# Performance work log

Measured on AMD Instinct MI355X. Metric: run time of the kernel, lower is better.

## Reference

```python
import jax, jax.numpy as jnp
import numpy as np

B, L, C = 256, 196, 768      # batch, tokens (14x14 grid), token_dim
K = 2048                      # codebook size (num_tokens)
H = W = 14                    # h = int(sqrt(L)), w = L // h


def setup_inputs() -> dict:
    key = jax.random.key(0)
    k1, k2, k3 = jax.random.split(key, 3)
    in_feas = jax.random.normal(k1, (B, L, C), dtype=jnp.float32)
    codebook = jax.random.normal(k2, (K, C), dtype=jnp.float32)
    # Conv1d(in=C, out=1, kernel=3, padding=1, bias=False) weight: [1, C, 3]
    att_w = jax.random.normal(k3, (1, C, 3), dtype=jnp.float32) * 0.02
    return {"in_feas": in_feas, "codebook": codebook, "att_w": att_w}


def reference(in_feas, codebook, att_w):
    b, l, c = in_feas.shape
    flat = in_feas.reshape(-1, c)  # [B*L, C]

    # --- SOHO visual-dictionary (VQ) nearest-neighbour lookup ---
    d = (jnp.sum(flat * flat, axis=1, keepdims=True)
         - 2.0 * flat @ codebook.T
         + jnp.sum(codebook * codebook, axis=1)[None, :])  # [B*L, K]
    encoding_indices = jnp.argmin(d, axis=1)               # [B*L] int
    quantized = codebook[encoding_indices]                 # [B*L, C]
    # straight-through estimator: output = x + sg(q - x)
    vd_outputs = flat + jax.lax.stop_gradient(quantized - flat)

    idx_out = encoding_indices.reshape(-1, H, W)

    # --- attention branch (att=True, not_plus=False) ---
    # Conv1d(C->1, k=3, pad=1) applied to each token as a length-1 sequence:
    # only the center tap att_w[0, :, 1] multiplies real data (neighbors are
    # zero padding), so the conv reduces to a dot with the center weights.
    att = jax.nn.relu(vd_outputs @ att_w[0, :, 1])         # [B*L]
    att_mask = jax.nn.softmax(att.reshape(b, l, 1), axis=1)  # softmax over L

    vd_outputs = vd_outputs.reshape(b, l, c)
    out_feas = vd_outputs + in_feas * att_mask
    return out_feas, idx_out
```

## Files before the change

kernel.cpp:

```cpp
#include <hip/hip_runtime.h>

#define B_ 256
#define L_ 196
#define C_ 768
#define K_ 2048
#define BL_ 50176

typedef __attribute__((ext_vector_type(8))) short bf16x8;
typedef __attribute__((ext_vector_type(4))) float f32x4;

typedef const __attribute__((address_space(1))) void gas_void;
typedef __attribute__((address_space(3))) void las_void;

__device__ __forceinline__ unsigned short f2bf(float f) {
  unsigned u = __builtin_bit_cast(unsigned, f);
  u = u + 0x7FFFu + ((u >> 16) & 1u);
  return (unsigned short)(u >> 16);
}

__device__ __forceinline__ unsigned fmono(float f) {
  unsigned u = __builtin_bit_cast(unsigned, f);
  return u ^ ((unsigned)((int)u >> 31) | 0x80000000u);
}

__global__ __launch_bounds__(256) void precompute_kernel(
    const float* __restrict__ cb, const float* __restrict__ attw,
    unsigned short* __restrict__ cbb, double* __restrict__ norms64,
    float* __restrict__ norms32, float* __restrict__ ac) {
  int wave = threadIdx.x >> 6;
  int lane = threadIdx.x & 63;
  int k = blockIdx.x * 4 + wave;
  const float* row = cb + (size_t)k * C_;
  double n = 0.0, a = 0.0;
  for (int c = lane; c < C_; c += 64) {
    float v = row[c];
    cbb[(size_t)k * C_ + c] = f2bf(v);
    n = fma((double)v, (double)v, n);
    a = fma((double)v, (double)attw[c * 3 + 1], a);
  }
  for (int off = 32; off > 0; off >>= 1) {
    n += __shfl_down(n, off);
    a += __shfl_down(a, off);
  }
  if (lane == 0) {
    norms64[k] = n;
    norms32[k] = (float)n;
    ac[k] = (a > 0.0) ? (float)a : 0.0f;
  }
}

__global__ __launch_bounds__(256) void convert_kernel(
    const float* __restrict__ x, unsigned short* __restrict__ xb) {
  int i = blockIdx.x * 256 + threadIdx.x;
  float4 v = ((const float4*)x)[i];
  uint2 w;
  w.x = (unsigned)f2bf(v.x) | ((unsigned)f2bf(v.y) << 16);
  w.y = (unsigned)f2bf(v.z) | ((unsigned)f2bf(v.w) << 16);
  ((uint2*)xb)[i] = w;
}

__global__ __launch_bounds__(256) void phase1_kernel(
    const unsigned short* __restrict__ xb,
    const unsigned short* __restrict__ cbb,
    const float* __restrict__ norms32, unsigned* __restrict__ ws_cand) {
  __shared__ unsigned short As[128 * 64];
  __shared__ unsigned short Bs[128 * 64];
  __shared__ float norms_s[128];
  __shared__ unsigned cands_s[128][8];

  int tid = threadIdx.x;
  int mblk = blockIdx.x, nblk = blockIdx.y;
  size_t row0 = (size_t)mblk * 128;
  int code0 = nblk * 128;

  if (tid < 128) norms_s[tid] = norms32[code0 + tid];

  int w = tid >> 6, l = tid & 63;
  int wm = w >> 1, wn = w & 1;
  int col16 = l & 15, quad = l >> 4;

  f32x4 acc[4][4];
#pragma unroll
  for (int mt = 0; mt < 4; ++mt)
#pragma unroll
    for (int nt = 0; nt < 4; ++nt) acc[mt][nt] = (f32x4){0.f, 0.f, 0.f, 0.f};

  int srow = 32 * w + (l >> 3);
  int sslot = (l & 7) ^ (l >> 3);
  const unsigned short* asrc = xb + (row0 + srow) * (size_t)C_ + sslot * 8;
  const unsigned short* bsrc =
      cbb + (size_t)(code0 + srow) * C_ + sslot * 8;
  char* alds = (char*)As + w * 4096;
  char* blds = (char*)Bs + w * 4096;

  for (int kt = 0; kt < 12; ++kt) {
    __syncthreads();
    int koff = kt * 64;
#pragma unroll
    for (int i = 0; i < 4; ++i) {
      __builtin_amdgcn_global_load_lds((gas_void*)(asrc + koff + i * 8 * C_),
                                       (las_void*)(alds + i * 1024), 16, 0, 0);
      __builtin_amdgcn_global_load_lds((gas_void*)(bsrc + koff + i * 8 * C_),
                                       (las_void*)(blds + i * 1024), 16, 0, 0);
    }
    __syncthreads();
#pragma unroll
    for (int ks = 0; ks < 2; ++ks) {
      int slot = (ks * 4 + quad) ^ (col16 & 7);
      bf16x8 af[4], bf[4];
#pragma unroll
      for (int mt = 0; mt < 4; ++mt) {
        int row = wm * 64 + mt * 16 + col16;
        af[mt] = *(const bf16x8*)((const char*)As + row * 128 + slot * 16);
      }
#pragma unroll
      for (int nt = 0; nt < 4; ++nt) {
        int row = wn * 64 + nt * 16 + col16;
        bf[nt] = *(const bf16x8*)((const char*)Bs + row * 128 + slot * 16);
      }
#pragma unroll
      for (int mt = 0; mt < 4; ++mt)
#pragma unroll
        for (int nt = 0; nt < 4; ++nt)
          acc[mt][nt] = __builtin_amdgcn_mfma_f32_16x16x32_bf16(
              af[mt], bf[nt], acc[mt][nt], 0, 0, 0);
    }
  }

#pragma unroll
  for (int mt = 0; mt < 4; ++mt) {
#pragma unroll
    for (int r = 0; r < 4; ++r) {
      unsigned keys[4];
#pragma unroll
      for (int nt = 0; nt < 4; ++nt) {
        int codel = wn * 64 + nt * 16 + col16;
        float d = fmaf(-2.0f, acc[mt][nt][r], norms_s[codel]);
        keys[nt] = (fmono(d) & 0xFFFFF800u) | (unsigned)(code0 + codel);
      }
      unsigned win[3];
#pragma unroll
      for (int rnd = 0; rnd < 3; ++rnd) {
        unsigned mn = min(min(keys[0], keys[1]), min(keys[2], keys[3]));
        mn = min(mn, (unsigned)__shfl_xor((int)mn, 1));
        mn = min(mn, (unsigned)__shfl_xor((int)mn, 2));
        mn = min(mn, (unsigned)__shfl_xor((int)mn, 4));
        mn = min(mn, (unsigned)__shfl_xor((int)mn, 8));
        win[rnd] = mn;
#pragma unroll
        for (int nt = 0; nt < 4; ++nt)
          if (keys[nt] == mn) keys[nt] = 0xFFFFFFFFu;
      }
      if (col16 == 0) {
        int t = wm * 64 + mt * 16 + quad * 4 + r;
        cands_s[t][wn * 3 + 0] = win[0];
        cands_s[t][wn * 3 + 1] = win[1];
        cands_s[t][wn * 3 + 2] = win[2];
      }
    }
  }
  __syncthreads();
  for (int i = tid; i < 128 * 6; i += 256) {
    int t = i / 6;
    int j = i - t * 6;
    ws_cand[(row0 + t) * 96 + nblk * 6 + j] = cands_s[t][j];
  }
}

__global__ __launch_bounds__(256) void phase2_kernel(
    const float* __restrict__ x, const float* __restrict__ cb,
    const unsigned* __restrict__ ws_cand, const double* __restrict__ norms64,
    int* __restrict__ out_idx) {
  __shared__ unsigned cl[32][100];
  __shared__ int rcode[32][6];
  __shared__ double rd[32][6];
  int tid = threadIdx.x;
  size_t tok0 = (size_t)blockIdx.x * 32;

  for (int i = tid; i < 32 * 96; i += 256) {
    int t = i / 96;
    int s = i - t * 96;
    cl[t][s] = ws_cand[tok0 * 96 + i];
  }
  __syncthreads();

  if (tid < 32) {
    unsigned best[6];
#pragma unroll
    for (int j = 0; j < 6; ++j) best[j] = 0xFFFFFFFFu;
    for (int s = 0; s < 96; ++s) {
      unsigned v = cl[tid][s];
      if (v < best[5]) {
        best[5] = v;
#pragma unroll
        for (int j = 5; j > 0; --j) {
          if (best[j] < best[j - 1]) {
            unsigned t = best[j];
            best[j] = best[j - 1];
            best[j - 1] = t;
          }
        }
      }
    }
#pragma unroll
    for (int j = 0; j < 6; ++j) rcode[tid][j] = (int)(best[j] & 0x7FFu);
  }
  __syncthreads();

  if (tid < 192) {
    int t = tid / 6;
    int j = tid - t * 6;
    int code = rcode[t][j];
    const float* xr = x + (tok0 + t) * (size_t)C_;
    const float* cr = cb + (size_t)code * C_;
    double s = 0.0;
    for (int c = 0; c < C_; c += 4) {
      float4 xa = *(const float4*)(xr + c);
      float4 ca = *(const float4*)(cr + c);
      s = fma((double)xa.x, (double)ca.x, s);
      s = fma((double)xa.y, (double)ca.y, s);
      s = fma((double)xa.z, (double)ca.z, s);
      s = fma((double)xa.w, (double)ca.w, s);
    }
    rd[t][j] = fma(-2.0, s, norms64[code]);
  }
  __syncthreads();

  if (tid < 32) {
    double bv = rd[tid][0];
    int bi = rcode[tid][0];
#pragma unroll
    for (int j = 1; j < 6; ++j) {
      double v = rd[tid][j];
      int i0 = rcode[tid][j];
      if (v < bv || (v == bv && i0 < bi)) {
        bv = v;
        bi = i0;
      }
    }
    out_idx[tok0 + tid] = bi;
  }
}

#define APAD 776
__global__ __launch_bounds__(256, 2) void argmin_fallback(
    const float* __restrict__ x, const float* __restrict__ cb,
    const unsigned short* __restrict__ cbb,
    const double* __restrict__ norms64, const float* __restrict__ norms32,
    int* __restrict__ out_idx) {
  __shared__ unsigned short Asf[32 * APAD];
  __shared__ float norms_s[K_];
  __shared__ unsigned int cands[32][48];
  __shared__ int rcode[32][6];
  __shared__ double rd[32][6];

  int tid = threadIdx.x;
  size_t tok0 = (size_t)blockIdx.x * 32;

  for (int i = tid; i < K_; i += 256) norms_s[i] = norms32[i];

  const float4* xin = (const float4*)(x + tok0 * C_);
  for (int i = tid; i < 32 * 192; i += 256) {
    int tok = i / 192;
    int c4 = i - tok * 192;
    float4 v = xin[i];
    uint2 w;
    w.x = (unsigned)f2bf(v.x) | ((unsigned)f2bf(v.y) << 16);
    w.y = (unsigned)f2bf(v.z) | ((unsigned)f2bf(v.w) << 16);
    *(uint2*)&Asf[tok * APAD + c4 * 4] = w;
  }
  __syncthreads();

  int wv = tid >> 6;
  int lane = tid & 63;
  int col = lane & 15;
  int quad = lane >> 4;

  const unsigned short* a0p = &Asf[(col)*APAD + quad * 8];
  const unsigned short* a1p = &Asf[(16 + col) * APAD + quad * 8];

  for (int chunk = 0; chunk < 4; ++chunk) {
    int code0 = chunk * 512 + wv * 128 + col;
    const unsigned short* bbase = cbb + (size_t)code0 * C_ + quad * 8;

    f32x4 acc[2][8];
#pragma unroll
    for (int m = 0; m < 2; ++m)
#pragma unroll
      for (int n = 0; n < 8; ++n) acc[m][n] = (f32x4){0.f, 0.f, 0.f, 0.f};

    bf16x8 ca0 = *(const bf16x8*)(a0p);
    bf16x8 ca1 = *(const bf16x8*)(a1p);
    bf16x8 cbf[8];
#pragma unroll
    for (int n = 0; n < 8; ++n)
      cbf[n] = *(const bf16x8*)(bbase + (size_t)n * 16 * C_);

    for (int ks = 0; ks < 24; ++ks) {
      bf16x8 na0, na1, nbf[8];
      if (ks < 23) {
        int k1 = (ks + 1) * 32;
        na0 = *(const bf16x8*)(a0p + k1);
        na1 = *(const bf16x8*)(a1p + k1);
#pragma unroll
        for (int n = 0; n < 8; ++n)
          nbf[n] = *(const bf16x8*)(bbase + (size_t)n * 16 * C_ + k1);
      }
#pragma unroll
      for (int n = 0; n < 8; ++n) {
        acc[0][n] = __builtin_amdgcn_mfma_f32_16x16x32_bf16(ca0, cbf[n],
                                                            acc[0][n], 0, 0, 0);
        acc[1][n] = __builtin_amdgcn_mfma_f32_16x16x32_bf16(ca1, cbf[n],
                                                            acc[1][n], 0, 0, 0);
      }
      if (ks < 23) {
        ca0 = na0;
        ca1 = na1;
#pragma unroll
        for (int n = 0; n < 8; ++n) cbf[n] = nbf[n];
      }
    }

#pragma unroll
    for (int m = 0; m < 2; ++m) {
#pragma unroll
      for (int r = 0; r < 4; ++r) {
        unsigned keys[8];
#pragma unroll
        for (int n = 0; n < 8; ++n) {
          int code = code0 + n * 16;
          float d = fmaf(-2.0f, acc[m][n][r], norms_s[code]);
          keys[n] = (fmono(d) & 0xFFFFF800u) | (unsigned)code;
        }
        unsigned win[3];
#pragma unroll
        for (int rnd = 0; rnd < 3; ++rnd) {
          unsigned mn = keys[0];
#pragma unroll
          for (int n = 1; n < 8; ++n) mn = min(mn, keys[n]);
          mn = min(mn, (unsigned)__shfl_xor((int)mn, 1));
          mn = min(mn, (unsigned)__shfl_xor((int)mn, 2));
          mn = min(mn, (unsigned)__shfl_xor((int)mn, 4));
          mn = min(mn, (unsigned)__shfl_xor((int)mn, 8));
          win[rnd] = mn;
#pragma unroll
          for (int n = 0; n < 8; ++n)
            if (keys[n] == mn) keys[n] = 0xFFFFFFFFu;
        }
        if (col == 0) {
          int token = m * 16 + quad * 4 + r;
          unsigned* cp = &cands[token][chunk * 12 + wv * 3];
          cp[0] = win[0];
          cp[1] = win[1];
          cp[2] = win[2];
        }
      }
    }
  }
  __syncthreads();

  if (tid < 32) {
    unsigned best[6];
#pragma unroll
    for (int j = 0; j < 6; ++j) best[j] = 0xFFFFFFFFu;
    for (int s = 0; s < 48; ++s) {
      unsigned v = cands[tid][s];
      if (v < best[5]) {
        best[5] = v;
#pragma unroll
        for (int j = 5; j > 0; --j) {
          if (best[j] < best[j - 1]) {
            unsigned t = best[j];
            best[j] = best[j - 1];
            best[j - 1] = t;
          }
        }
      }
    }
#pragma unroll
    for (int j = 0; j < 6; ++j) rcode[tid][j] = (int)(best[j] & 0x7FFu);
  }
  __syncthreads();

  if (tid < 192) {
    int t = tid / 6;
    int j = tid - t * 6;
    int code = rcode[t][j];
    const float* xr = x + (tok0 + t) * (size_t)C_;
    const float* cr = cb + (size_t)code * C_;
    double s = 0.0;
    for (int c = 0; c < C_; c += 4) {
      float4 xa = *(const float4*)(xr + c);
      float4 ca = *(const float4*)(cr + c);
      s = fma((double)xa.x, (double)ca.x, s);
      s = fma((double)xa.y, (double)ca.y, s);
      s = fma((double)xa.z, (double)ca.z, s);
      s = fma((double)xa.w, (double)ca.w, s);
    }
    rd[t][j] = fma(-2.0, s, norms64[code]);
  }
  __syncthreads();

  if (tid < 32) {
    double bv = rd[tid][0];
    int bi = rcode[tid][0];
#pragma unroll
    for (int j = 1; j < 6; ++j) {
      double v = rd[tid][j];
      int i0 = rcode[tid][j];
      if (v < bv || (v == bv && i0 < bi)) {
        bv = v;
        bi = i0;
      }
    }
    out_idx[tok0 + tid] = bi;
  }
}

__global__ __launch_bounds__(256) void epilogue_kernel(
    const float* __restrict__ x, const float* __restrict__ cb,
    const float* __restrict__ ac, const int* __restrict__ idx,
    float* __restrict__ out, float* __restrict__ out_idx) {
  __shared__ float att[256];
  __shared__ float red[256];
  __shared__ int ids[L_];
  int b = blockIdx.x;
  int tid = threadIdx.x;

  float a = -1e30f;
  int myid = 0;
  if (tid < L_) {
    myid = idx[b * L_ + tid];
    ids[tid] = myid;
    a = ac[myid];
  }
  att[tid] = a;
  red[tid] = a;
  __syncthreads();
  for (int s = 128; s > 0; s >>= 1) {
    if (tid < s) red[tid] = fmaxf(red[tid], red[tid + s]);
    __syncthreads();
  }
  float m = red[0];
  __syncthreads();
  float e = (tid < L_) ? expf(att[tid] - m) : 0.0f;
  red[tid] = e;
  __syncthreads();
  for (int s = 128; s > 0; s >>= 1) {
    if (tid < s) red[tid] += red[tid + s];
    __syncthreads();
  }
  float sum = red[0];
  __syncthreads();
  att[tid] = e / sum;
  __syncthreads();

  const float4* xin = (const float4*)(x + (size_t)b * L_ * C_);
  float4* o = (float4*)(out + (size_t)b * L_ * C_);
  for (int i = tid; i < L_ * (C_ / 4); i += 256) {
    int l = i / (C_ / 4);
    int c4 = i - l * (C_ / 4);
    const float4* crow = (const float4*)(cb + (size_t)ids[l] * C_);
    float4 xv = xin[i];
    float4 cv = crow[c4];
    float mk = att[l];
    float4 ov;
    ov.x = cv.x + xv.x * mk;
    ov.y = cv.y + xv.y * mk;
    ov.z = cv.z + xv.z * mk;
    ov.w = cv.w + xv.w * mk;
    o[i] = ov;
  }
  if (tid < L_) out_idx[b * L_ + tid] = (float)ids[tid];
}

extern "C" void kernel_launch(void* const* d_in, const int* in_sizes, int n_in,
                              void* d_out, int out_size, void* d_ws,
                              size_t ws_size, hipStream_t stream) {
  const float* in_feas = (const float*)d_in[0];
  const float* cb = (const float*)d_in[1];
  const float* attw = (const float*)d_in[2];

  char* ws = (char*)d_ws;
  size_t off = 0;
  unsigned short* cbb = (unsigned short*)(ws + off); off += 3145728;
  double* norms64 = (double*)(ws + off);           off += 16384;
  float* norms32 = (float*)(ws + off);             off += 8192;
  float* ac = (float*)(ws + off);                  off += 8192;
  int* idx = (int*)(ws + off);                     off += 200704;
  size_t base = off;
  unsigned short* xb = (unsigned short*)(ws + off); off += (size_t)BL_ * C_ * 2;
  unsigned* ws_cand = (unsigned*)(ws + off);        off += (size_t)BL_ * 96 * 4;
  size_t need_full = off;

  float* out = (float*)d_out;
  float* out_idx = out + (size_t)B_ * L_ * C_;

  precompute_kernel<<<K_ / 4, 256, 0, stream>>>(cb, attw, cbb, norms64,
                                                norms32, ac);
  if (ws_size >= need_full) {
    convert_kernel<<<BL_ * C_ / 4 / 256, 256, 0, stream>>>(in_feas, xb);
    dim3 g1(BL_ / 128, K_ / 128);
    phase1_kernel<<<g1, 256, 0, stream>>>(xb, cbb, norms32, ws_cand);
    phase2_kernel<<<BL_ / 32, 256, 0, stream>>>(in_feas, cb, ws_cand, norms64,
                                                idx);
  } else {
    argmin_fallback<<<BL_ / 32, 256, 0, stream>>>(in_feas, cb, cbb, norms64,
                                                  norms32, idx);
  }
  epilogue_kernel<<<B_, 256, 0, stream>>>(in_feas, cb, ac, idx, out, out_idx);
  (void)base;
}
```

Measured before the change: 785.2 us.

## Enlarge phase1 GEMM tile to 256x256 with double-buffered LDS prefetch

Phase1 now uses 512-thread blocks computing 256x256 tiles (8x4 MFMA tiles per wave) and double-buffers the A/B LDS stages, so the next k-slice loads while the current one is multiplied and only one barrier runs per iteration. A 1D grid with the code block in the low bits of the block id makes consecutive blocks share the same token rows. The larger tile raises operand reuse and cuts the number of blocks. In exchange it needs 128KB of LDS and many more accumulator registers, which can limit occupancy.

```diff
diff --git a/kernel.cpp b/kernel.cpp
--- a/kernel.cpp
+++ b/kernel.cpp
@@ -59,76 +59,90 @@
   ((uint2*)xb)[i] = w;
 }
 
-__global__ __launch_bounds__(256) void phase1_kernel(
+__global__ __launch_bounds__(512, 2) void phase1_kernel(
     const unsigned short* __restrict__ xb,
     const unsigned short* __restrict__ cbb,
     const float* __restrict__ norms32, unsigned* __restrict__ ws_cand) {
-  __shared__ unsigned short As[128 * 64];
-  __shared__ unsigned short Bs[128 * 64];
-  __shared__ float norms_s[128];
-  __shared__ unsigned cands_s[128][8];
+  __shared__ unsigned short As[2][256 * 64];
+  __shared__ unsigned short Bs[2][256 * 64];
+  __shared__ float norms_s[256];
+  __shared__ unsigned cands_s[256][12];
 
   int tid = threadIdx.x;
-  int mblk = blockIdx.x, nblk = blockIdx.y;
-  size_t row0 = (size_t)mblk * 128;
-  int code0 = nblk * 128;
-
-  if (tid < 128) norms_s[tid] = norms32[code0 + tid];
+  int bid = blockIdx.x;
+  int nblk = bid & 7;
+  int mblk = bid >> 3;
+  size_t row0 = (size_t)mblk * 256;
+  int code0 = nblk * 256;
 
   int w = tid >> 6, l = tid & 63;
-  int wm = w >> 1, wn = w & 1;
+  int wm = w >> 2, wn = w & 3;
   int col16 = l & 15, quad = l >> 4;
 
-  f32x4 acc[4][4];
-#pragma unroll
-  for (int mt = 0; mt < 4; ++mt)
+  if (tid < 256) norms_s[tid] = norms32[code0 + tid];
+
+  int crow = tid >> 3;
+  int slotraw = (tid & 7) ^ (crow & 7);
+  size_t off0 = (size_t)crow * C_ + (size_t)slotraw * 8;
+  const unsigned short* abase = xb + row0 * C_ + off0;
+  const unsigned short* bbase = cbb + (size_t)code0 * C_ + off0;
+  char* alds = (char*)&As[0][0] + w * 1024;
+  char* blds = (char*)&Bs[0][0] + w * 1024;
+
+  auto stage = [&](int kt, int buf) {
+    const unsigned short* a_ = abase + kt * 64;
+    const unsigned short* b_ = bbase + kt * 64;
+    char* al_ = alds + buf * 32768;
+    char* bl_ = blds + buf * 32768;
+#pragma unroll
+    for (int i = 0; i < 4; ++i) {
+      __builtin_amdgcn_global_load_lds((gas_void*)(a_ + (size_t)i * 64 * C_),
+                                       (las_void*)(al_ + i * 8192), 16, 0, 0);
+      __builtin_amdgcn_global_load_lds((gas_void*)(b_ + (size_t)i * 64 * C_),
+                                       (las_void*)(bl_ + i * 8192), 16, 0, 0);
+    }
+  };
+
+  f32x4 acc[8][4];
+#pragma unroll
+  for (int mt = 0; mt < 8; ++mt)
 #pragma unroll
     for (int nt = 0; nt < 4; ++nt) acc[mt][nt] = (f32x4){0.f, 0.f, 0.f, 0.f};
 
-  int srow = 32 * w + (l >> 3);
-  int sslot = (l & 7) ^ (l >> 3);
-  const unsigned short* asrc = xb + (row0 + srow) * (size_t)C_ + sslot * 8;
-  const unsigned short* bsrc =
-      cbb + (size_t)(code0 + srow) * C_ + sslot * 8;
-  char* alds = (char*)As + w * 4096;
-  char* blds = (char*)Bs + w * 4096;
+  stage(0, 0);
+  __syncthreads();
 
   for (int kt = 0; kt < 12; ++kt) {
-    __syncthreads();
-    int koff = kt * 64;
-#pragma unroll
-    for (int i = 0; i < 4; ++i) {
-      __builtin_amdgcn_global_load_lds((gas_void*)(asrc + koff + i * 8 * C_),
-                                       (las_void*)(alds + i * 1024), 16, 0, 0);
-      __builtin_amdgcn_global_load_lds((gas_void*)(bsrc + koff + i * 8 * C_),
-                                       (las_void*)(blds + i * 1024), 16, 0, 0);
-    }
-    __syncthreads();
+    int buf = kt & 1;
+    if (kt < 11) stage(kt + 1, buf ^ 1);
+    const char* Ab = (const char*)&As[buf][0];
+    const char* Bb = (const char*)&Bs[buf][0];
 #pragma unroll
     for (int ks = 0; ks < 2; ++ks) {
-      int slot = (ks * 4 + quad) ^ (col16 & 7);
-      bf16x8 af[4], bf[4];
-#pragma unroll
-      for (int mt = 0; mt < 4; ++mt) {
-        int row = wm * 64 + mt * 16 + col16;
-        af[mt] = *(const bf16x8*)((const char*)As + row * 128 + slot * 16);
+      int sl = (ks * 4 + quad) ^ (col16 & 7);
+      bf16x8 af[8], bf[4];
+#pragma unroll
+      for (int mt = 0; mt < 8; ++mt) {
+        int row = wm * 128 + mt * 16 + col16;
+        af[mt] = *(const bf16x8*)(Ab + row * 128 + sl * 16);
       }
 #pragma unroll
       for (int nt = 0; nt < 4; ++nt) {
         int row = wn * 64 + nt * 16 + col16;
-        bf[nt] = *(const bf16x8*)((const char*)Bs + row * 128 + slot * 16);
-      }
-#pragma unroll
-      for (int mt = 0; mt < 4; ++mt)
+        bf[nt] = *(const bf16x8*)(Bb + row * 128 + sl * 16);
+      }
+#pragma unroll
+      for (int mt = 0; mt < 8; ++mt)
 #pragma unroll
         for (int nt = 0; nt < 4; ++nt)
           acc[mt][nt] = __builtin_amdgcn_mfma_f32_16x16x32_bf16(
               af[mt], bf[nt], acc[mt][nt], 0, 0, 0);
     }
-  }
-
-#pragma unroll
-  for (int mt = 0; mt < 4; ++mt) {
+    __syncthreads();
+  }
+
+#pragma unroll
+  for (int mt = 0; mt < 8; ++mt) {
 #pragma unroll
     for (int r = 0; r < 4; ++r) {
       unsigned keys[4];
@@ -152,7 +166,7 @@
           if (keys[nt] == mn) keys[nt] = 0xFFFFFFFFu;
       }
       if (col16 == 0) {
-        int t = wm * 64 + mt * 16 + quad * 4 + r;
+        int t = wm * 128 + mt * 16 + quad * 4 + r;
         cands_s[t][wn * 3 + 0] = win[0];
         cands_s[t][wn * 3 + 1] = win[1];
         cands_s[t][wn * 3 + 2] = win[2];
@@ -160,10 +174,10 @@
     }
   }
   __syncthreads();
-  for (int i = tid; i < 128 * 6; i += 256) {
-    int t = i / 6;
-    int j = i - t * 6;
-    ws_cand[(row0 + t) * 96 + nblk * 6 + j] = cands_s[t][j];
+  for (int i = tid; i < 256 * 12; i += 512) {
+    int t = i / 12;
+    int j = i - t * 12;
+    ws_cand[(row0 + t) * 96 + nblk * 12 + j] = cands_s[t][j];
   }
 }
 
@@ -500,8 +514,8 @@
                                                 norms32, ac);
   if (ws_size >= need_full) {
     convert_kernel<<<BL_ * C_ / 4 / 256, 256, 0, stream>>>(in_feas, xb);
-    dim3 g1(BL_ / 128, K_ / 128);
-    phase1_kernel<<<g1, 256, 0, stream>>>(xb, cbb, norms32, ws_cand);
+    phase1_kernel<<<dim3((BL_ / 256) * (K_ / 256)), 512, 0, stream>>>(
+        xb, cbb, norms32, ws_cand);
     phase2_kernel<<<BL_ / 32, 256, 0, stream>>>(in_feas, cb, ws_cand, norms64,
                                                 idx);
   } else {
```

After: 804.9 us. 2.5% more time.
